# Kernel optimization log

Measured on AMD Instinct MI355X. Metric: run time of the kernel, lower is better.

Reference implementation:

```python
import jax, jax.numpy as jnp
import numpy as np

N = 50000          # nodes
E = 1_600_000      # edges
IN_DIM = 64
HID = 64
HEADS = 2
EDGE_DIM = 8
OUT_DIM = 2
NEG_SLOPE = 0.2    # PyG GATConv default negative_slope


def _gat_params(key, in_ch, out_ch, heads, edge_dim, concat):
    ks = jax.random.split(key, 6)
    s = 0.1
    W = jax.random.normal(ks[0], (in_ch, heads * out_ch), jnp.float32) * s
    a_src = jax.random.normal(ks[1], (heads, out_ch), jnp.float32) * s
    a_dst = jax.random.normal(ks[2], (heads, out_ch), jnp.float32) * s
    We = jax.random.normal(ks[3], (edge_dim, heads * out_ch), jnp.float32) * s
    a_e = jax.random.normal(ks[4], (heads, out_ch), jnp.float32) * s
    b = jnp.zeros((heads * out_ch if concat else out_ch,), jnp.float32)
    return W, a_src, a_dst, We, a_e, b


def gat_conv(x, edge_index, edge_attr, W, a_src, a_dst, We, a_e, b, heads, out_ch, concat):
    # Faithful PyG GATConv with edge_dim, add_self_loops=True, fill_value='mean'.
    n = x.shape[0]
    src0, dst0 = edge_index[0], edge_index[1]
    # self-loop edge_attr = mean of incoming edge attrs (scatter-mean over dst)
    cnt = jax.ops.segment_sum(jnp.ones((src0.shape[0],), x.dtype), dst0, num_segments=n)
    loop_attr = jax.ops.segment_sum(edge_attr, dst0, num_segments=n) / jnp.maximum(cnt, 1.0)[:, None]
    loop = jnp.arange(n, dtype=src0.dtype)
    src = jnp.concatenate([src0, loop])
    dst = jnp.concatenate([dst0, loop])
    ea = jnp.concatenate([edge_attr, loop_attr], axis=0)          # [E+N, edge_dim]

    h = (x @ W).reshape(n, heads, out_ch)                          # [N, H, C]
    al_src = jnp.einsum('nhc,hc->nh', h, a_src)                    # [N, H]
    al_dst = jnp.einsum('nhc,hc->nh', h, a_dst)
    e = (ea @ We).reshape(-1, heads, out_ch)                       # [E+N, H, C]
    al_edge = jnp.einsum('ehc,hc->eh', e, a_e)

    alpha = jax.nn.leaky_relu(al_src[src] + al_dst[dst] + al_edge, NEG_SLOPE)  # [E+N, H]
    # segment softmax over destination node (every dst has a self loop)
    amax = jax.ops.segment_max(alpha, dst, num_segments=n)
    ex = jnp.exp(alpha - amax[dst])
    denom = jax.ops.segment_sum(ex, dst, num_segments=n)
    w = ex / (denom[dst] + 1e-16)

    out = jax.ops.segment_sum(h[src] * w[:, :, None], dst, num_segments=n)     # [N, H, C]
    out = out.reshape(n, heads * out_ch) if concat else out.mean(axis=1)
    return out + b


def setup_inputs() -> dict:
    key = jax.random.key(0)
    ks = jax.random.split(key, 8)
    inp = {
        'x': jax.random.normal(ks[0], (N, IN_DIM), jnp.float32),
        'edge_index': jax.random.randint(ks[1], (2, E), 0, N, dtype=jnp.int32),
        'edge_attr': jax.random.normal(ks[2], (E, EDGE_DIM), jnp.float32),
    }
    # layer 0: in -> hid, heads=1, concat=True
    for name, p in zip(['W0', 'as0', 'ad0', 'We0', 'ae0', 'b0'], _gat_params(ks[3], IN_DIM, HID, 1, EDGE_DIM, True)):
        inp[name] = p
    # layers 1,2: hid -> hid, heads=HEADS, concat=False
    for name, p in zip(['W1', 'as1', 'ad1', 'We1', 'ae1', 'b1'], _gat_params(ks[4], HID, HID, HEADS, EDGE_DIM, False)):
        inp[name] = p
    for name, p in zip(['W2', 'as2', 'ad2', 'We2', 'ae2', 'b2'], _gat_params(ks[5], HID, HID, HEADS, EDGE_DIM, False)):
        inp[name] = p
    # final: hid -> out_dim, heads=1, concat=True
    for name, p in zip(['W3', 'as3', 'ad3', 'We3', 'ae3', 'b3'], _gat_params(ks[6], HID, OUT_DIM, 1, EDGE_DIM, True)):
        inp[name] = p
    return inp


def reference(x, edge_index, edge_attr,
              W0, as0, ad0, We0, ae0, b0,
              W1, as1, ad1, We1, ae1, b1,
              W2, as2, ad2, We2, ae2, b2,
              W3, as3, ad3, We3, ae3, b3):
    h = jax.nn.relu(gat_conv(x, edge_index, edge_attr, W0, as0, ad0, We0, ae0, b0, 1, HID, True))
    h = jax.nn.relu(gat_conv(h, edge_index, edge_attr, W1, as1, ad1, We1, ae1, b1, HEADS, HID, False))
    h = jax.nn.relu(gat_conv(h, edge_index, edge_attr, W2, as2, ad2, We2, ae2, b2, HEADS, HID, False))
    return gat_conv(h, edge_index, edge_attr, W3, as3, ad3, We3, ae3, b3, 1, OUT_DIM, True)
```

## Files before the change

### kernel.cpp

```cpp
#include <hip/hip_runtime.h>
#include <math.h>


#define GSZ 256
#define CAPB 10240
#define CHUNK 4096
#define CAP_C 9984

__device__ __forceinline__ float wave_sum64(float v) {
#pragma unroll
  for (int o = 32; o >= 1; o >>= 1) v += __shfl_xor(v, o);
  return v;
}
__device__ __forceinline__ float dot8(const float4& a, const float4& b,
                                      const float* c) {
  return a.x * c[0] + a.y * c[1] + a.z * c[2] + a.w * c[3] + b.x * c[4] +
         b.y * c[5] + b.z * c[6] + b.w * c[7];
}


__global__ __launch_bounds__(256) void bin_kernel(const int* __restrict__ src,
                                                  const int* __restrict__ dst,
                                                  int* __restrict__ bfill,
                                                  int2* __restrict__ bbuf,
                                                  int E_) {
  __shared__ int histo[256];
  __shared__ int scanb[256];
  __shared__ int segstart[256];
  __shared__ int gbase[256];
  __shared__ int cur[256];
  __shared__ int2 stage[CHUNK];
  __shared__ int gtarg[CHUNK];
  const int t = threadIdx.x;
  const int e0 = blockIdx.x * CHUNK;
  const int cnt = min(CHUNK, E_ - e0);
  histo[t] = 0;
  __syncthreads();
  int myd[CHUNK / 256];
#pragma unroll
  for (int k = 0; k < CHUNK / 256; ++k) {
    int i = t + k * 256;
    int d = -1;
    if (i < cnt) {
      d = dst[e0 + i];
      atomicAdd(&histo[d >> 8], 1);
    }
    myd[k] = d;
  }
  __syncthreads();
  const int v = histo[t];
  int acc = v;
  scanb[t] = v;
  __syncthreads();
#pragma unroll
  for (int o = 1; o < 256; o <<= 1) {
    int u = (t >= o) ? scanb[t - o] : 0;
    __syncthreads();
    acc += u;
    scanb[t] = acc;
    __syncthreads();
  }
  int gp = 0;
  if (v > 0) gp = atomicAdd(&bfill[t], v);
  segstart[t] = acc - v;
  gbase[t] = t * CAPB + min(gp, CAPB - v);
  cur[t] = 0;
  __syncthreads();
#pragma unroll
  for (int k = 0; k < CHUNK / 256; ++k) {
    int i = t + k * 256;
    int d = myd[k];
    if (d >= 0) {
      int b = d >> 8;
      int s = src[e0 + i];
      int p = atomicAdd(&cur[b], 1);
      int sl = segstart[b] + p;
      stage[sl] = make_int2(s, (e0 + i) | ((d & 255) << 21));
      gtarg[sl] = gbase[b] + p;
    }
  }
  __syncthreads();
  for (int i = t; i < cnt; i += 256) bbuf[gtarg[i]] = stage[i];
}

__global__ __launch_bounds__(256) void count_kernel(
    const int* __restrict__ bfill, const int2* __restrict__ bbuf,
    int* __restrict__ cnt, int n) {
  __shared__ int h[256];
  const int b = blockIdx.x;
  const int t = threadIdx.x;
  h[t] = 0;
  __syncthreads();
  const int m = min(bfill[b], CAPB);
  const int2* reg = bbuf + (size_t)b * CAPB;
  for (int i = t; i < m; i += 256) {
    int dl = ((unsigned)reg[i].y) >> 21;
    atomicAdd(&h[dl], 1);
  }
  __syncthreads();
  int node = b * GSZ + t;
  if (node < n) cnt[node] = h[t];
}

__global__ __launch_bounds__(256) void scan1_kernel(const int* __restrict__ cnt,
                                                    int* __restrict__ rowp,
                                                    int* __restrict__ bsum,
                                                    int n) {
  __shared__ int sd[256];
  const int t = threadIdx.x;
  const int base = blockIdx.x * 1024 + t * 4;
  int v0 = (base + 0 < n) ? cnt[base + 0] + 1 : 0;
  int v1 = (base + 1 < n) ? cnt[base + 1] + 1 : 0;
  int v2 = (base + 2 < n) ? cnt[base + 2] + 1 : 0;
  int v3 = (base + 3 < n) ? cnt[base + 3] + 1 : 0;
  const int s = v0 + v1 + v2 + v3;
  sd[t] = s;
  __syncthreads();
  int acc = s;
#pragma unroll
  for (int o = 1; o < 256; o <<= 1) {
    int u = (t >= o) ? sd[t - o] : 0;
    __syncthreads();
    acc += u;
    sd[t] = acc;
    __syncthreads();
  }
  int excl = acc - s;
  if (base + 0 < n) rowp[base + 0] = excl;
  if (base + 1 < n) rowp[base + 1] = excl + v0;
  if (base + 2 < n) rowp[base + 2] = excl + v0 + v1;
  if (base + 3 < n) rowp[base + 3] = excl + v0 + v1 + v2;
  if (t == 255) bsum[blockIdx.x] = acc;
}

__global__ void scan2_kernel(int* __restrict__ bsum, int nb) {
  const int lane = threadIdx.x;
  int v = (lane < nb) ? bsum[lane] : 0;
  int incl = v;
#pragma unroll
  for (int o = 1; o < 64; o <<= 1) {
    int u = __shfl_up(incl, o);
    if (lane >= o) incl += u;
  }
  if (lane < nb) bsum[lane] = incl - v;
  if (lane == 63) bsum[nb] = incl;
}

__global__ void scan3_kernel(int* __restrict__ rowp,
                             const int* __restrict__ bsum, int n, int nb) {
  int i = blockIdx.x * 256 + threadIdx.x;
  if (i >= n) return;
  rowp[i] += bsum[i >> 10];
  if (i == 0) rowp[n] = bsum[nb];
}

__global__ __launch_bounds__(256) void place_kernel(
    const int* __restrict__ rowp, const int* __restrict__ bfill,
    const int2* __restrict__ bbuf, int* __restrict__ col_src,
    int* __restrict__ eidA, int n, int E_) {
  __shared__ int rp[GSZ + 1];
  __shared__ int cur[GSZ];
  __shared__ int2 stage[CAP_C];
  const int b = blockIdx.x;
  const int t = threadIdx.x;
  const int lo = b * GSZ;
  const int nk = min(GSZ, n - lo);
  for (int i = t; i <= nk; i += 256) rp[i] = rowp[lo + i];
  cur[t] = 0;
  __syncthreads();
  const int s0 = rp[0];
  const int span = rp[nk] - s0;
  const bool fits = (span <= CAP_C);
  const int m = min(bfill[b], CAPB);
  const int2* reg = bbuf + (size_t)b * CAPB;
  for (int i = t; i < m; i += 256) {
    int2 pl = reg[i];
    int dl = ((unsigned)pl.y) >> 21;
    int e2 = pl.y & 0x1FFFFF;
    int p = atomicAdd(&cur[dl], 1);
    int slot = rp[dl] + p;
    if (fits) stage[slot - s0] = make_int2(pl.x, e2);
    else { col_src[slot] = pl.x; eidA[slot] = e2; }
  }
  if (t < nk) {
    int slot = rp[t + 1] - 1;
    int node = lo + t;
    if (fits) stage[slot - s0] = make_int2(node, E_ + node);
    else { col_src[slot] = node; eidA[slot] = E_ + node; }
  }
  __syncthreads();
  if (fits) {
    for (int i = t; i < span; i += 256) {
      int2 v = stage[i];
      col_src[s0 + i] = v.x;
      eidA[s0 + i] = v.y;
    }
  }
}

__global__ void comb_all_kernel(const float* __restrict__ We0,
                                const float* __restrict__ ae0,
                                const float* __restrict__ We1,
                                const float* __restrict__ ae1,
                                const float* __restrict__ We2,
                                const float* __restrict__ ae2,
                                const float* __restrict__ We3,
                                const float* __restrict__ ae3,
                                float* __restrict__ comb) {
  int t = threadIdx.x;
  if (t >= 48) return;
  float s = 0.f;
  if (t < 8) {
    int d = t;
    for (int c = 0; c < 64; ++c) s += We0[d * 64 + c] * ae0[c];
  } else if (t < 24) {
    int idx = t - 8, h = idx >> 3, d = idx & 7;
    for (int c = 0; c < 64; ++c) s += We1[d * 128 + h * 64 + c] * ae1[h * 64 + c];
  } else if (t < 40) {
    int idx = t - 24, h = idx >> 3, d = idx & 7;
    for (int c = 0; c < 64; ++c) s += We2[d * 128 + h * 64 + c] * ae2[h * 64 + c];
  } else {
    int d = t - 40;
    for (int c = 0; c < 2; ++c) s += We3[d * 2 + c] * ae3[c];
  }
  comb[t] = s;
}

__global__ __launch_bounds__(256) void edge_prep_kernel(
    const int* __restrict__ row_ptr, const int* __restrict__ eid,
    const float* __restrict__ ea, const float* __restrict__ comb,
    float* __restrict__ edot0, float* __restrict__ e1a,
    float* __restrict__ e1b, float* __restrict__ e2a,
    float* __restrict__ e2b, float* __restrict__ edot3, int n, int E_) {
  __shared__ float cb[48];
  if (threadIdx.x < 48) cb[threadIdx.x] = comb[threadIdx.x];
  __syncthreads();
  const int lane = threadIdx.x & 63;
  const int node = blockIdx.x * 4 + (threadIdx.x >> 6);
  if (node >= n) return;

  const int start = row_ptr[node];
  const int selfpos = row_ptr[node + 1] - 1;

  float s0 = 0.f, s1 = 0.f, s2 = 0.f, s3 = 0.f, s4 = 0.f, s5 = 0.f, s6 = 0.f,
        s7 = 0.f;
  for (int i = start + lane; i < selfpos; i += 64) {
    int id = eid[i];
    const float4* v = reinterpret_cast<const float4*>(ea + (size_t)id * 8);
    float4 a = v[0], b = v[1];
    s0 += a.x; s1 += a.y; s2 += a.z; s3 += a.w;
    s4 += b.x; s5 += b.y; s6 += b.z; s7 += b.w;
    edot0[i] = dot8(a, b, cb + 0);
    e1a[i] = dot8(a, b, cb + 8);
    e1b[i] = dot8(a, b, cb + 16);
    e2a[i] = dot8(a, b, cb + 24);
    e2b[i] = dot8(a, b, cb + 32);
    edot3[i] = dot8(a, b, cb + 40);
  }
#pragma unroll
  for (int o = 32; o >= 1; o >>= 1) {
    s0 += __shfl_xor(s0, o); s1 += __shfl_xor(s1, o);
    s2 += __shfl_xor(s2, o); s3 += __shfl_xor(s3, o);
    s4 += __shfl_xor(s4, o); s5 += __shfl_xor(s5, o);
    s6 += __shfl_xor(s6, o); s7 += __shfl_xor(s7, o);
  }
  if (lane == 0) {
    float deg = (float)(selfpos - start);
    float inv = 1.f / fmaxf(deg, 1.f);
    float4 a = make_float4(s0 * inv, s1 * inv, s2 * inv, s3 * inv);
    float4 b = make_float4(s4 * inv, s5 * inv, s6 * inv, s7 * inv);
    int i = selfpos;
    edot0[i] = dot8(a, b, cb + 0);
    e1a[i] = dot8(a, b, cb + 8);
    e1b[i] = dot8(a, b, cb + 16);
    e2a[i] = dot8(a, b, cb + 24);
    e2b[i] = dot8(a, b, cb + 32);
    edot3[i] = dot8(a, b, cb + 40);
  }
}

template <int HC, int H>
__global__ __launch_bounds__(256) void gemm_proj_kernel(
    const float* __restrict__ x, const float* __restrict__ W,
    const float* __restrict__ a_src, const float* __restrict__ a_dst,
    float* __restrict__ h, float* __restrict__ al_src,
    float* __restrict__ al_dst, int n) {
  constexpr int IN = 64;
  constexpr int C = HC / H;
  __shared__ float xs[32][IN];
  const int tid = threadIdx.x;
  const int j = tid % HC;
  const int rsub = tid / HC;
  constexpr int RPP = 256 / HC > 0 ? 256 / HC : 1;

  float wr[IN];
#pragma unroll
  for (int k = 0; k < IN; ++k) wr[k] = W[k * HC + j];
  const float asj = a_src[j];
  const float adj = a_dst[j];

  const int row0 = blockIdx.x * 32;
  {
    const float4* xv = reinterpret_cast<const float4*>(x);
    float4* xsv = reinterpret_cast<float4*>(&xs[0][0]);
    for (int i = tid; i < 32 * IN / 4; i += 256) {
      int r = i / (IN / 4);
      int row = row0 + r;
      float4 v = make_float4(0.f, 0.f, 0.f, 0.f);
      if (row < n) v = xv[(size_t)row * (IN / 4) + (i % (IN / 4))];
      xsv[i] = v;
    }
  }
  __syncthreads();

  for (int rb = 0; rb < 32; rb += RPP) {
    int r = rb + rsub;
    if (r >= 32) break;
    int row = row0 + r;
    float acc = 0.f;
#pragma unroll
    for (int k4 = 0; k4 < IN / 4; ++k4) {
      float4 xv = *reinterpret_cast<const float4*>(&xs[r][k4 * 4]);
      acc += xv.x * wr[k4 * 4 + 0] + xv.y * wr[k4 * 4 + 1] +
             xv.z * wr[k4 * 4 + 2] + xv.w * wr[k4 * 4 + 3];
    }
    if (row < n) {
      size_t oidx = (H == 2)
                        ? ((size_t)(j >> 6) * ((size_t)n * 64) +
                           (size_t)row * 64 + (j & 63))
                        : ((size_t)row * HC + j);
      h[oidx] = acc;
    }
    float ps = acc * asj;
    float pd = acc * adj;
#pragma unroll
    for (int o = C / 2; o >= 1; o >>= 1) {
      ps += __shfl_xor(ps, o);
      pd += __shfl_xor(pd, o);
    }
    if (row < n && (j % C) == 0) {
      int hh = j / C;
      al_src[(size_t)hh * n + row] = ps;
      al_dst[(size_t)hh * n + row] = pd;
    }
  }
}

template <int C, bool RELU>
__global__ __launch_bounds__(256) void gat_node_kernel(
    const int* __restrict__ row_ptr, const int* __restrict__ col_src,
    const float* __restrict__ edot, const float* __restrict__ h_proj,
    const float* __restrict__ al_src, const float* __restrict__ al_dst,
    const float* __restrict__ bias, float* __restrict__ out, int n) {
  const int lane = threadIdx.x & 63;
  const int node = blockIdx.x * 4 + (threadIdx.x >> 6);
  if (node >= n) return;

  const float adn = al_dst[node];
  const int start = row_ptr[node];
  const int end = row_ptr[node + 1];

  float denp = 0.f;
  float4 acc4 = make_float4(0.f, 0.f, 0.f, 0.f);
  float accp = 0.f;

  const int sub = lane & 15;
  const int grp16 = lane >> 4;

  for (int base = start; base < end; base += 64) {
    const int i = base + lane;
    const bool valid = (i < end);
    int s = 0;
    float ex = 0.f;
    if (valid) {
      s = col_src[i];
      float a = al_src[s] + adn + edot[i];
      a = (a > 0.f) ? a : 0.2f * a;
      ex = __expf(a);
    }
    denp += ex;

    const int cntc = min(64, end - base);
    if (C == 2) {
      const int half = lane >> 1;
      const int ch = lane & 1;
#pragma unroll
      for (int sb = 0; sb < 2; ++sb) {
        int tt = sb * 32 + half;
        int sv = __shfl(s, tt);
        float w = __shfl(ex, tt);
        if (tt < cntc) accp += w * h_proj[sv * 2 + ch];
      }
    } else {
      auto issue = [&](int g, float4 (&v)[4], float (&w)[4]) {
#pragma unroll
        for (int u = 0; u < 4; ++u) {
          int tt = (g * 4 + u) * 4 + grp16;
          int sv = __shfl(s, tt);
          w[u] = __shfl(ex, tt);
          v[u] = *reinterpret_cast<const float4*>(h_proj + (size_t)sv * 64 +
                                                  sub * 4);
        }
      };
      auto fma4 = [&](float4 (&v)[4], float (&w)[4]) {
#pragma unroll
        for (int u = 0; u < 4; ++u) {
          acc4.x += w[u] * v[u].x; acc4.y += w[u] * v[u].y;
          acc4.z += w[u] * v[u].z; acc4.w += w[u] * v[u].w;
        }
      };
      const int nbat = (cntc + 15) >> 4;
      float4 va[4], vb[4];
      float wa[4], wb[4];
      issue(0, va, wa);
      int g = 0;
      for (;;) {
        if (g + 1 < nbat) issue(g + 1, vb, wb);
        fma4(va, wa);
        if (++g >= nbat) break;
        if (g + 1 < nbat) issue(g + 1, va, wa);
        fma4(vb, wb);
        if (++g >= nbat) break;
      }
    }
  }

  const float den = wave_sum64(denp);

  if (C == 2) {
#pragma unroll
    for (int o = 2; o <= 32; o <<= 1) accp += __shfl_xor(accp, o);
    if (lane < 2) {
      float v = accp / (den + 1e-16f) + bias[lane];
      if (RELU) v = fmaxf(v, 0.f);
      out[node * 2 + lane] = v;
    }
  } else {
    acc4.x += __shfl_xor(acc4.x, 16); acc4.x += __shfl_xor(acc4.x, 32);
    acc4.y += __shfl_xor(acc4.y, 16); acc4.y += __shfl_xor(acc4.y, 32);
    acc4.z += __shfl_xor(acc4.z, 16); acc4.z += __shfl_xor(acc4.z, 32);
    acc4.w += __shfl_xor(acc4.w, 16); acc4.w += __shfl_xor(acc4.w, 32);
    if (lane < 16) {
      float inv = 1.f / (den + 1e-16f);
      float4 bv = *reinterpret_cast<const float4*>(bias + sub * 4);
      float4 o;
      o.x = acc4.x * inv + bv.x; o.y = acc4.y * inv + bv.y;
      o.z = acc4.z * inv + bv.z; o.w = acc4.w * inv + bv.w;
      if (RELU) {
        o.x = fmaxf(o.x, 0.f); o.y = fmaxf(o.y, 0.f);
        o.z = fmaxf(o.z, 0.f); o.w = fmaxf(o.w, 0.f);
      }
      *reinterpret_cast<float4*>(out + (size_t)node * 64 + sub * 4) = o;
    }
  }
}

template <bool FIRST>
__global__ __launch_bounds__(256) void gat_head_kernel(
    const int* __restrict__ row_ptr, const int* __restrict__ col_src,
    const float* __restrict__ edotH, const float* __restrict__ hplane,
    const float* __restrict__ al_srcH, const float* __restrict__ al_dstH,
    const float* __restrict__ bias, float* __restrict__ partial,
    float* __restrict__ out, int n) {
  const int lane = threadIdx.x & 63;
  const int node = blockIdx.x * 4 + (threadIdx.x >> 6);
  if (node >= n) return;

  const float adn = al_dstH[node];
  const int start = row_ptr[node];
  const int end = row_ptr[node + 1];

  float denp = 0.f;
  float4 acc4 = make_float4(0.f, 0.f, 0.f, 0.f);

  const int sub = lane & 15;
  const int grp16 = lane >> 4;

  for (int base = start; base < end; base += 64) {
    const int i = base + lane;
    const bool valid = (i < end);
    int s = 0;
    float ex = 0.f;
    if (valid) {
      s = col_src[i];
      float a = al_srcH[s] + adn + edotH[i];
      a = (a > 0.f) ? a : 0.2f * a;
      ex = __expf(a);
    }
    denp += ex;

    const int cntc = min(64, end - base);
    auto issue = [&](int g, float4 (&v)[4], float (&w)[4]) {
#pragma unroll
      for (int u = 0; u < 4; ++u) {
        int tt = (g * 4 + u) * 4 + grp16;
        int sv = __shfl(s, tt);
        w[u] = __shfl(ex, tt);
        v[u] = *reinterpret_cast<const float4*>(hplane + (size_t)sv * 64 +
                                                sub * 4);
      }
    };
    auto fma4 = [&](float4 (&v)[4], float (&w)[4]) {
#pragma unroll
      for (int u = 0; u < 4; ++u) {
        acc4.x += w[u] * v[u].x; acc4.y += w[u] * v[u].y;
        acc4.z += w[u] * v[u].z; acc4.w += w[u] * v[u].w;
      }
    };
    const int nbat = (cntc + 15) >> 4;
    float4 va[4], vb[4];
    float wa[4], wb[4];
    issue(0, va, wa);
    int g = 0;
    for (;;) {
      if (g + 1 < nbat) issue(g + 1, vb, wb);
      fma4(va, wa);
      if (++g >= nbat) break;
      if (g + 1 < nbat) issue(g + 1, va, wa);
      fma4(vb, wb);
      if (++g >= nbat) break;
    }
  }

  const float den = wave_sum64(denp);

  acc4.x += __shfl_xor(acc4.x, 16); acc4.x += __shfl_xor(acc4.x, 32);
  acc4.y += __shfl_xor(acc4.y, 16); acc4.y += __shfl_xor(acc4.y, 32);
  acc4.z += __shfl_xor(acc4.z, 16); acc4.z += __shfl_xor(acc4.z, 32);
  acc4.w += __shfl_xor(acc4.w, 16); acc4.w += __shfl_xor(acc4.w, 32);
  if (lane < 16) {
    float inv = 1.f / (den + 1e-16f);
    if (FIRST) {
      float4 o;
      o.x = acc4.x * inv; o.y = acc4.y * inv;
      o.z = acc4.z * inv; o.w = acc4.w * inv;
      *reinterpret_cast<float4*>(partial + (size_t)node * 64 + sub * 4) = o;
    } else {
      float4 p =
          *reinterpret_cast<const float4*>(partial + (size_t)node * 64 + sub * 4);
      float4 bv = *reinterpret_cast<const float4*>(bias + sub * 4);
      float4 o;
      o.x = fmaxf((p.x + acc4.x * inv) * 0.5f + bv.x, 0.f);
      o.y = fmaxf((p.y + acc4.y * inv) * 0.5f + bv.y, 0.f);
      o.z = fmaxf((p.z + acc4.z * inv) * 0.5f + bv.z, 0.f);
      o.w = fmaxf((p.w + acc4.w * inv) * 0.5f + bv.w, 0.f);
      *reinterpret_cast<float4*>(out + (size_t)node * 64 + sub * 4) = o;
    }
  }
}


static inline size_t align_up(size_t v, size_t a) { return (v + a - 1) & ~(a - 1); }

extern "C" void kernel_launch(void* const* d_in, const int* in_sizes, int n_in,
                              void* d_out, int out_size, void* d_ws,
                              size_t ws_size, hipStream_t stream) {
  const float* x = (const float*)d_in[0];
  const int* ei = (const int*)d_in[1];
  const float* ea = (const float*)d_in[2];

  const int N = in_sizes[0] / 64;
  const int E = in_sizes[1] / 2;
  const int* src0 = ei;
  const int* dst0 = ei + E;
  const int M = E + N;

  const float* W[4] = {(const float*)d_in[3], (const float*)d_in[9],
                       (const float*)d_in[15], (const float*)d_in[21]};
  const float* As[4] = {(const float*)d_in[4], (const float*)d_in[10],
                        (const float*)d_in[16], (const float*)d_in[22]};
  const float* Ad[4] = {(const float*)d_in[5], (const float*)d_in[11],
                        (const float*)d_in[17], (const float*)d_in[23]};
  const float* We[4] = {(const float*)d_in[6], (const float*)d_in[12],
                        (const float*)d_in[18], (const float*)d_in[24]};
  const float* Ae[4] = {(const float*)d_in[7], (const float*)d_in[13],
                        (const float*)d_in[19], (const float*)d_in[25]};
  const float* B[4] = {(const float*)d_in[8], (const float*)d_in[14],
                       (const float*)d_in[20], (const float*)d_in[26]};

  char* p = (char*)d_ws;
  size_t off = 0;
  auto carve = [&](size_t bytes) {
    void* r = p + off;
    off = align_up(off + bytes, 256);
    return r;
  };
  const int NBK = (N + GSZ - 1) / GSZ;
  int* cnt = (int*)carve((size_t)N * 4);
  int* row_ptr = (int*)carve((size_t)(N + 1) * 4);
  int* bsum = (int*)carve((size_t)256 * 4);
  int* bfill = (int*)carve((size_t)NBK * 4);
  int2* bbuf = (int2*)carve((size_t)NBK * CAPB * 8);
  int* col_src = (int*)carve((size_t)M * 4);
  int* eid = (int*)carve((size_t)M * 4);
  float* comb = (float*)carve(256);
  float* edot0 = (float*)carve((size_t)M * 4);
  float* e1a = (float*)carve((size_t)M * 4);
  float* e1b = (float*)carve((size_t)M * 4);
  float* e2a = (float*)carve((size_t)M * 4);
  float* e2b = (float*)carve((size_t)M * 4);
  float* edot3 = (float*)carve((size_t)M * 4);
  float* al_src = (float*)carve((size_t)N * 2 * 4);
  float* al_dst = (float*)carve((size_t)N * 2 * 4);
  float* h_proj = (float*)carve((size_t)N * 128 * 4);
  float* buf_a = (float*)carve((size_t)N * 64 * 4);
  float* buf_b = (float*)carve((size_t)N * 64 * 4);
  float* partial = (float*)bbuf;
  (void)ws_size;

  const int nb = (N + 1023) / 1024;

  hipMemsetAsync(bfill, 0, (size_t)NBK * 4, stream);
  bin_kernel<<<(E + CHUNK - 1) / CHUNK, 256, 0, stream>>>(src0, dst0, bfill,
                                                          bbuf, E);
  count_kernel<<<NBK, 256, 0, stream>>>(bfill, bbuf, cnt, N);
  scan1_kernel<<<nb, 256, 0, stream>>>(cnt, row_ptr, bsum, N);
  scan2_kernel<<<1, 64, 0, stream>>>(bsum, nb);
  scan3_kernel<<<(N + 255) / 256, 256, 0, stream>>>(row_ptr, bsum, N, nb);
  place_kernel<<<NBK, 256, 0, stream>>>(row_ptr, bfill, bbuf, col_src, eid, N,
                                        E);
  comb_all_kernel<<<1, 64, 0, stream>>>(We[0], Ae[0], We[1], Ae[1], We[2],
                                        Ae[2], We[3], Ae[3], comb);
  edge_prep_kernel<<<(N + 3) / 4, 256, 0, stream>>>(
      row_ptr, eid, ea, comb, edot0, e1a, e1b, e2a, e2b, edot3, N, E);

  const int gemm_grid = (N + 31) / 32;
  const int node_grid = (N + 3) / 4;
  const size_t plane = (size_t)N * 64;

  gemm_proj_kernel<64, 1><<<gemm_grid, 256, 0, stream>>>(
      x, W[0], As[0], Ad[0], h_proj, al_src, al_dst, N);
  gat_node_kernel<64, true><<<node_grid, 256, 0, stream>>>(
      row_ptr, col_src, edot0, h_proj, al_src, al_dst, B[0], buf_a, N);

  gemm_proj_kernel<128, 2><<<gemm_grid, 256, 0, stream>>>(
      buf_a, W[1], As[1], Ad[1], h_proj, al_src, al_dst, N);
  gat_head_kernel<true><<<node_grid, 256, 0, stream>>>(
      row_ptr, col_src, e1a, h_proj, al_src, al_dst, B[1], partial, nullptr, N);
  gat_head_kernel<false><<<node_grid, 256, 0, stream>>>(
      row_ptr, col_src, e1b, h_proj + plane, al_src + N, al_dst + N, B[1],
      partial, buf_b, N);

  gemm_proj_kernel<128, 2><<<gemm_grid, 256, 0, stream>>>(
      buf_b, W[2], As[2], Ad[2], h_proj, al_src, al_dst, N);
  gat_head_kernel<true><<<node_grid, 256, 0, stream>>>(
      row_ptr, col_src, e2a, h_proj, al_src, al_dst, B[2], partial, nullptr, N);
  gat_head_kernel<false><<<node_grid, 256, 0, stream>>>(
      row_ptr, col_src, e2b, h_proj + plane, al_src + N, al_dst + N, B[2],
      partial, buf_a, N);

  gemm_proj_kernel<2, 1><<<gemm_grid, 256, 0, stream>>>(
      buf_a, W[3], As[3], Ad[3], h_proj, al_src, al_dst, N);
  gat_node_kernel<2, false><<<node_grid, 256, 0, stream>>>(
      row_ptr, col_src, edot3, h_proj, al_src, al_dst, B[3], (float*)d_out, N);
}
```

Baseline: 475.5 us.

## Flatten edge-prep over node blocks and compute self-loop terms from per-edge dots

Replaces the one-wave-per-node edge prep with a kernel that handles 128 nodes per block and walks their contiguous edge span with all threads, so low-degree nodes no longer leave most lanes idle. The self-loop attention term is now the mean of the per-edge dot products, using linearity, and is computed serially by one thread per node that re-reads the just-written outputs. The placement step keeps the packed local-node bits in eid, and the prep kernel masks them off. The serial per-node loop adds imbalance for high-degree nodes, and the block-level sync and re-read rely on global writes being visible within the block.

Result: slower. 526.4 us (+10.7%).

```diff
diff --git a/kernel.cpp b/kernel.cpp
--- a/kernel.cpp
+++ b/kernel.cpp
@@ -6,6 +6,7 @@
 #define CAPB 10240
 #define CHUNK 4096
 #define CAP_C 9984
+#define NPB 128
 
 __device__ __forceinline__ float wave_sum64(float v) {
 #pragma unroll
@@ -176,17 +177,17 @@
   for (int i = t; i < m; i += 256) {
     int2 pl = reg[i];
     int dl = ((unsigned)pl.y) >> 21;
-    int e2 = pl.y & 0x1FFFFF;
     int p = atomicAdd(&cur[dl], 1);
     int slot = rp[dl] + p;
-    if (fits) stage[slot - s0] = make_int2(pl.x, e2);
-    else { col_src[slot] = pl.x; eidA[slot] = e2; }
+    if (fits) stage[slot - s0] = pl;
+    else { col_src[slot] = pl.x; eidA[slot] = pl.y; }
   }
   if (t < nk) {
     int slot = rp[t + 1] - 1;
     int node = lo + t;
-    if (fits) stage[slot - s0] = make_int2(node, E_ + node);
-    else { col_src[slot] = node; eidA[slot] = E_ + node; }
+    int pv = (E_ + node) | (t << 21);
+    if (fits) stage[slot - s0] = make_int2(node, pv);
+    else { col_src[slot] = node; eidA[slot] = pv; }
   }
   __syncthreads();
   if (fits) {
@@ -226,56 +227,60 @@
   comb[t] = s;
 }
 
-__global__ __launch_bounds__(256) void edge_prep_kernel(
-    const int* __restrict__ row_ptr, const int* __restrict__ eid,
+__global__ __launch_bounds__(256) void edge_prep2_kernel(
+    const int* __restrict__ rowp, const int* __restrict__ eid,
     const float* __restrict__ ea, const float* __restrict__ comb,
     float* __restrict__ edot0, float* __restrict__ e1a,
     float* __restrict__ e1b, float* __restrict__ e2a,
     float* __restrict__ e2b, float* __restrict__ edot3, int n, int E_) {
   __shared__ float cb[48];
-  if (threadIdx.x < 48) cb[threadIdx.x] = comb[threadIdx.x];
-  __syncthreads();
-  const int lane = threadIdx.x & 63;
-  const int node = blockIdx.x * 4 + (threadIdx.x >> 6);
-  if (node >= n) return;
-
-  const int start = row_ptr[node];
-  const int selfpos = row_ptr[node + 1] - 1;
-
-  float s0 = 0.f, s1 = 0.f, s2 = 0.f, s3 = 0.f, s4 = 0.f, s5 = 0.f, s6 = 0.f,
-        s7 = 0.f;
-  for (int i = start + lane; i < selfpos; i += 64) {
-    int id = eid[i];
-    const float4* v = reinterpret_cast<const float4*>(ea + (size_t)id * 8);
-    float4 a = v[0], b = v[1];
-    s0 += a.x; s1 += a.y; s2 += a.z; s3 += a.w;
-    s4 += b.x; s5 += b.y; s6 += b.z; s7 += b.w;
-    edot0[i] = dot8(a, b, cb + 0);
-    e1a[i] = dot8(a, b, cb + 8);
-    e1b[i] = dot8(a, b, cb + 16);
-    e2a[i] = dot8(a, b, cb + 24);
-    e2b[i] = dot8(a, b, cb + 32);
-    edot3[i] = dot8(a, b, cb + 40);
-  }
-#pragma unroll
-  for (int o = 32; o >= 1; o >>= 1) {
-    s0 += __shfl_xor(s0, o); s1 += __shfl_xor(s1, o);
-    s2 += __shfl_xor(s2, o); s3 += __shfl_xor(s3, o);
-    s4 += __shfl_xor(s4, o); s5 += __shfl_xor(s5, o);
-    s6 += __shfl_xor(s6, o); s7 += __shfl_xor(s7, o);
-  }
-  if (lane == 0) {
-    float deg = (float)(selfpos - start);
-    float inv = 1.f / fmaxf(deg, 1.f);
-    float4 a = make_float4(s0 * inv, s1 * inv, s2 * inv, s3 * inv);
-    float4 b = make_float4(s4 * inv, s5 * inv, s6 * inv, s7 * inv);
-    int i = selfpos;
-    edot0[i] = dot8(a, b, cb + 0);
-    e1a[i] = dot8(a, b, cb + 8);
-    e1b[i] = dot8(a, b, cb + 16);
-    e2a[i] = dot8(a, b, cb + 24);
-    e2b[i] = dot8(a, b, cb + 32);
-    edot3[i] = dot8(a, b, cb + 40);
+  __shared__ int rp[NPB + 1];
+  const int t = threadIdx.x;
+  if (t < 48) cb[t] = comb[t];
+  const int lo = blockIdx.x * NPB;
+  const int nk = min(NPB, n - lo);
+  for (int i = t; i <= nk; i += 256) rp[i] = rowp[lo + i];
+  __syncthreads();
+  const int s0 = rp[0];
+  const int span = rp[nk] - s0;
+
+  for (int i = t; i < span; i += 256) {
+    int v = eid[s0 + i];
+    int e = v & 0x1FFFFF;
+    if (e < E_) {
+      const float4* p = reinterpret_cast<const float4*>(ea + (size_t)e * 8);
+      float4 a = p[0], b = p[1];
+      int slot = s0 + i;
+      edot0[slot] = dot8(a, b, cb + 0);
+      e1a[slot] = dot8(a, b, cb + 8);
+      e1b[slot] = dot8(a, b, cb + 16);
+      e2a[slot] = dot8(a, b, cb + 24);
+      e2b[slot] = dot8(a, b, cb + 32);
+      edot3[slot] = dot8(a, b, cb + 40);
+    }
+  }
+  __syncthreads();
+
+  if (t < nk) {
+    const int a = rp[t];
+    const int b = rp[t + 1];
+    const int deg = b - 1 - a;
+    float s0s = 0.f, s1s = 0.f, s2s = 0.f, s3s = 0.f, s4s = 0.f, s5s = 0.f;
+    for (int j = a; j < b - 1; ++j) {
+      s0s += edot0[j];
+      s1s += e1a[j];
+      s2s += e1b[j];
+      s3s += e2a[j];
+      s4s += e2b[j];
+      s5s += edot3[j];
+    }
+    const float inv = 1.f / fmaxf((float)deg, 1.f);
+    edot0[b - 1] = s0s * inv;
+    e1a[b - 1] = s1s * inv;
+    e1b[b - 1] = s2s * inv;
+    e2a[b - 1] = s3s * inv;
+    e2b[b - 1] = s4s * inv;
+    edot3[b - 1] = s5s * inv;
   }
 }
 
@@ -621,7 +626,7 @@
                                         E);
   comb_all_kernel<<<1, 64, 0, stream>>>(We[0], Ae[0], We[1], Ae[1], We[2],
                                         Ae[2], We[3], Ae[3], comb);
-  edge_prep_kernel<<<(N + 3) / 4, 256, 0, stream>>>(
+  edge_prep2_kernel<<<(N + NPB - 1) / NPB, 256, 0, stream>>>(
       row_ptr, eid, ea, comb, edot0, e1a, e1b, e2a, e2b, edot3, N, E);
 
   const int gemm_grid = (N + 31) / 32;
```

## Split edge prep into flat per-edge dot kernel and self-loop mean kernel

Applied to the files above, without the earlier changes.

Replaces the per-node wave edge-prep kernel with a grid-stride per-edge kernel that computes the six attention dot products, plus a second per-node kernel that builds the self-loop values. The self-loop values are now the mean of the already-computed dots rather than dots of the mean attribute, which is valid because the dot is linear. This removes the load imbalance and idle lanes of one-wave-per-node processing on low-degree nodes. In exchange it adds a kernel launch and a second pass that re-reads the six dot arrays.

Result: slower. 491.3 us (+3.3%).

```diff
diff --git a/kernel.cpp b/kernel.cpp
--- a/kernel.cpp
+++ b/kernel.cpp
@@ -226,56 +226,52 @@
   comb[t] = s;
 }
 
-__global__ __launch_bounds__(256) void edge_prep_kernel(
-    const int* __restrict__ row_ptr, const int* __restrict__ eid,
-    const float* __restrict__ ea, const float* __restrict__ comb,
-    float* __restrict__ edot0, float* __restrict__ e1a,
-    float* __restrict__ e1b, float* __restrict__ e2a,
-    float* __restrict__ e2b, float* __restrict__ edot3, int n, int E_) {
+__global__ __launch_bounds__(256) void edge_dots_kernel(
+    const int* __restrict__ eid, const float* __restrict__ ea,
+    const float* __restrict__ comb, float* __restrict__ edot0,
+    float* __restrict__ e1a, float* __restrict__ e1b,
+    float* __restrict__ e2a, float* __restrict__ e2b,
+    float* __restrict__ edot3, int M_, int E_) {
   __shared__ float cb[48];
   if (threadIdx.x < 48) cb[threadIdx.x] = comb[threadIdx.x];
   __syncthreads();
+  const int stride = gridDim.x * 256;
+  for (int i = blockIdx.x * 256 + threadIdx.x; i < M_; i += stride) {
+    int e = eid[i];
+    if (e < E_) {
+      const float4* p = reinterpret_cast<const float4*>(ea + (size_t)e * 8);
+      float4 a = p[0], b = p[1];
+      edot0[i] = dot8(a, b, cb + 0);
+      e1a[i] = dot8(a, b, cb + 8);
+      e1b[i] = dot8(a, b, cb + 16);
+      e2a[i] = dot8(a, b, cb + 24);
+      e2b[i] = dot8(a, b, cb + 32);
+      edot3[i] = dot8(a, b, cb + 40);
+    }
+  }
+}
+
+__global__ __launch_bounds__(256) void self_mean_kernel(
+    const int* __restrict__ rowp, float* __restrict__ edot0,
+    float* __restrict__ e1a, float* __restrict__ e1b,
+    float* __restrict__ e2a, float* __restrict__ e2b,
+    float* __restrict__ edot3, int n) {
   const int lane = threadIdx.x & 63;
   const int node = blockIdx.x * 4 + (threadIdx.x >> 6);
   if (node >= n) return;
-
-  const int start = row_ptr[node];
-  const int selfpos = row_ptr[node + 1] - 1;
-
-  float s0 = 0.f, s1 = 0.f, s2 = 0.f, s3 = 0.f, s4 = 0.f, s5 = 0.f, s6 = 0.f,
-        s7 = 0.f;
-  for (int i = start + lane; i < selfpos; i += 64) {
-    int id = eid[i];
-    const float4* v = reinterpret_cast<const float4*>(ea + (size_t)id * 8);
-    float4 a = v[0], b = v[1];
-    s0 += a.x; s1 += a.y; s2 += a.z; s3 += a.w;
-    s4 += b.x; s5 += b.y; s6 += b.z; s7 += b.w;
-    edot0[i] = dot8(a, b, cb + 0);
-    e1a[i] = dot8(a, b, cb + 8);
-    e1b[i] = dot8(a, b, cb + 16);
-    e2a[i] = dot8(a, b, cb + 24);
-    e2b[i] = dot8(a, b, cb + 32);
-    edot3[i] = dot8(a, b, cb + 40);
-  }
-#pragma unroll
-  for (int o = 32; o >= 1; o >>= 1) {
-    s0 += __shfl_xor(s0, o); s1 += __shfl_xor(s1, o);
-    s2 += __shfl_xor(s2, o); s3 += __shfl_xor(s3, o);
-    s4 += __shfl_xor(s4, o); s5 += __shfl_xor(s5, o);
-    s6 += __shfl_xor(s6, o); s7 += __shfl_xor(s7, o);
-  }
+  const int a = rowp[node];
+  const int b = rowp[node + 1] - 1;
+  float s0 = 0.f, s1 = 0.f, s2 = 0.f, s3 = 0.f, s4 = 0.f, s5 = 0.f;
+  for (int j = a + lane; j < b; j += 64) {
+    s0 += edot0[j]; s1 += e1a[j]; s2 += e1b[j];
+    s3 += e2a[j]; s4 += e2b[j]; s5 += edot3[j];
+  }
+  s0 = wave_sum64(s0); s1 = wave_sum64(s1); s2 = wave_sum64(s2);
+  s3 = wave_sum64(s3); s4 = wave_sum64(s4); s5 = wave_sum64(s5);
   if (lane == 0) {
-    float deg = (float)(selfpos - start);
-    float inv = 1.f / fmaxf(deg, 1.f);
-    float4 a = make_float4(s0 * inv, s1 * inv, s2 * inv, s3 * inv);
-    float4 b = make_float4(s4 * inv, s5 * inv, s6 * inv, s7 * inv);
-    int i = selfpos;
-    edot0[i] = dot8(a, b, cb + 0);
-    e1a[i] = dot8(a, b, cb + 8);
-    e1b[i] = dot8(a, b, cb + 16);
-    e2a[i] = dot8(a, b, cb + 24);
-    e2b[i] = dot8(a, b, cb + 32);
-    edot3[i] = dot8(a, b, cb + 40);
+    float inv = 1.f / fmaxf((float)(b - a), 1.f);
+    edot0[b] = s0 * inv; e1a[b] = s1 * inv; e1b[b] = s2 * inv;
+    e2a[b] = s3 * inv; e2b[b] = s4 * inv; edot3[b] = s5 * inv;
   }
 }
 
@@ -621,8 +617,10 @@
                                         E);
   comb_all_kernel<<<1, 64, 0, stream>>>(We[0], Ae[0], We[1], Ae[1], We[2],
                                         Ae[2], We[3], Ae[3], comb);
-  edge_prep_kernel<<<(N + 3) / 4, 256, 0, stream>>>(
-      row_ptr, eid, ea, comb, edot0, e1a, e1b, e2a, e2b, edot3, N, E);
+  edge_dots_kernel<<<2048, 256, 0, stream>>>(eid, ea, comb, edot0, e1a, e1b,
+                                             e2a, e2b, edot3, M, E);
+  self_mean_kernel<<<(N + 3) / 4, 256, 0, stream>>>(row_ptr, edot0, e1a, e1b,
+                                                    e2a, e2b, edot3, N);
 
   const int gemm_grid = (N + 31) / 32;
   const int node_grid = (N + 3) / 4;
```
